# Optimization experiments

Measured on AMD Instinct MI355X. Metric: run time of the kernel, lower is better.

Reference implementation:

```python
import jax, jax.numpy as jnp
import numpy as np

D_IN = 1024
D_OUT = 1024
NUM_HEADS = 16
HEAD_DIM = D_OUT // NUM_HEADS
EPS = 1e-6
POW = 16.0


def setup_inputs() -> dict:
    key = jax.random.key(0)
    ks = jax.random.split(key, 6)
    s = 1.0 / np.sqrt(D_IN)
    x = jax.random.normal(ks[0], (2, 2048, D_IN), dtype=jnp.float32)
    Wq = jax.random.uniform(ks[1], (D_OUT, D_IN), jnp.float32, -s, s)
    Wk = jax.random.uniform(ks[2], (D_OUT, D_IN), jnp.float32, -s, s)
    Wv = jax.random.uniform(ks[3], (D_OUT, D_IN), jnp.float32, -s, s)
    Wo = jax.random.uniform(ks[4], (D_OUT, D_OUT), jnp.float32, -s, s)
    bo = jax.random.uniform(ks[5], (D_OUT,), jnp.float32, -s, s)
    return {"x": x, "Wq": Wq, "Wk": Wk, "Wv": Wv, "Wo": Wo, "bo": bo}


def _l2norm(t):
    # torch F.normalize: t / max(||t||, eps)
    n = jnp.sqrt(jnp.sum(t * t, axis=-1, keepdims=True))
    return t / jnp.maximum(n, EPS)


def reference(x, Wq, Wk, Wv, Wo, bo):
    B, T, _ = x.shape
    # project and split heads: [B, H, T, Dh]
    def heads(W):
        y = jnp.einsum('btd,od->bto', x, W)
        return y.reshape(B, T, NUM_HEADS, HEAD_DIM).transpose(0, 2, 1, 3)
    Q = _l2norm(heads(Wq))
    K = _l2norm(heads(Wk))
    V = heads(Wv)
    cos_sim = jnp.clip(jnp.einsum('bhtd,bhsd->bhts', Q, K), -0.999, 0.999)
    scores = 1.0 - jnp.arccos(cos_sim) / jnp.pi
    W = jnp.power(jnp.maximum(scores, EPS), POW)
    W = W / (jnp.sum(W, axis=-1, keepdims=True) + EPS)
    out = jnp.einsum('bhts,bhsd->bhtd', W, V)
    out = out.transpose(0, 2, 1, 3).reshape(B, T, D_OUT)
    return jnp.einsum('bto,po->btp', out, Wo) + bo
```

## Files before the change

### kernel.cpp

```cpp
#include <hip/hip_runtime.h>
#include <math.h>

constexpr int Dm   = 1024;
constexpr int NH   = 16;
constexpr int HD   = 64;
constexpr int Bb   = 2;
constexpr int Tt   = 2048;
constexpr int MTOT = Bb * Tt;
#define EPSF 1e-6f

typedef __attribute__((ext_vector_type(8))) short short8;
typedef __attribute__((ext_vector_type(4))) float f32x4;
typedef __attribute__((ext_vector_type(2))) float f32x2;

__device__ __forceinline__ ushort f2bf(float f) {
    union { float f; unsigned u; } v; v.f = f;
    unsigned r = (v.u + 0x7FFFu + ((v.u >> 16) & 1u)) >> 16;
    return (ushort)r;
}
__device__ __forceinline__ ushort f2bf_hu(float f) {
    return (ushort)((__builtin_bit_cast(unsigned, f) + 0x8000u) >> 16);
}

__device__ __forceinline__ void gload16(const void* g, void* l) {
    __builtin_amdgcn_global_load_lds(
        (const __attribute__((address_space(1))) unsigned int*)g,
        (__attribute__((address_space(3))) unsigned int*)l,
        16, 0, 0);
}

__global__ __launch_bounds__(256)
void cvt_all(const float* __restrict__ x,  const float* __restrict__ wq,
             const float* __restrict__ wk, const float* __restrict__ wv,
             const float* __restrict__ wo,
             ushort* __restrict__ xb,  ushort* __restrict__ wqb,
             ushort* __restrict__ wkb, ushort* __restrict__ wvb,
             ushort* __restrict__ wob) {
    int i = blockIdx.x * 256 + threadIdx.x;
    const float* src; ushort* dst; int off;
    if (i < 1048576)      { src = x;  dst = xb;  off = i; }
    else if (i < 1310720) { src = wq; dst = wqb; off = i - 1048576; }
    else if (i < 1572864) { src = wk; dst = wkb; off = i - 1310720; }
    else if (i < 1835008) { src = wv; dst = wvb; off = i - 1572864; }
    else                  { src = wo; dst = wob; off = i - 1835008; }
    const float4 v = ((const float4*)src)[off];
    ushort4 o;
    o.x = f2bf(v.x); o.y = f2bf(v.y); o.z = f2bf(v.z); o.w = f2bf(v.w);
    ((ushort4*)dst)[off] = o;
}

template<bool OUTF32>
__device__ __forceinline__
void gemm_core(const ushort* __restrict__ A, const ushort* __restrict__ W,
               const float* __restrict__ bias, void* __restrict__ out,
               int m0, int n0, int N, int K, int mode) {
    __shared__ ushort As[128 * 64];
    __shared__ ushort Bs[128 * 64];
    const int tid  = threadIdx.x;
    const int wave = tid >> 6, lane = tid & 63;
    const int quad = lane >> 4, l15 = lane & 15;
    const int wr = wave >> 1, wc = wave & 1;
    const int lr = lane >> 3;
    const int sc = (lane & 7) ^ lr;

    f32x4 acc[4][4] = {};
    const ushort* Ab = A + (size_t)(m0 + lr) * K + sc * 8;
    const ushort* Wb = W + (size_t)(n0 + lr) * K + sc * 8;

    for (int k0 = 0; k0 < K; k0 += 64) {
        #pragma unroll
        for (int i = 0; i < 4; i++) {
            const int rows8 = (wave * 4 + i) * 8;
            gload16(Ab + (size_t)rows8 * K + k0, &As[rows8 * 64]);
            gload16(Wb + (size_t)rows8 * K + k0, &Bs[rows8 * 64]);
        }
        __syncthreads();
        #pragma unroll
        for (int kh = 0; kh < 2; kh++) {
            short8 af[4];
            #pragma unroll
            for (int mi = 0; mi < 4; mi++) {
                const int row = wr * 64 + mi * 16 + l15;
                af[mi] = *(const short8*)&As[row * 64 + (((kh * 4 + quad) ^ (row & 7)) * 8)];
            }
            #pragma unroll
            for (int nj = 0; nj < 4; nj++) {
                const int row = wc * 64 + nj * 16 + l15;
                const short8 bf = *(const short8*)&Bs[row * 64 + (((kh * 4 + quad) ^ (row & 7)) * 8)];
                #pragma unroll
                for (int mi = 0; mi < 4; mi++)
                    acc[mi][nj] = __builtin_amdgcn_mfma_f32_16x16x32_bf16(af[mi], bf, acc[mi][nj], 0, 0, 0);
            }
        }
        __syncthreads();
    }

    if (!OUTF32 && mode == 2) {
        #pragma unroll
        for (int mi = 0; mi < 4; mi++) {
            const int t  = m0 + wr * 64 + mi * 16 + quad * 4;
            const int bb = t >> 11, tl = t & 2047;
            #pragma unroll
            for (int nj = 0; nj < 4; nj++) {
                const int n = n0 + wc * 64 + nj * 16 + l15;
                const int hh = n >> 6, dd = n & 63;
                uint2 pk;
                pk.x = (unsigned)f2bf(acc[mi][nj][0]) | ((unsigned)f2bf(acc[mi][nj][1]) << 16);
                pk.y = (unsigned)f2bf(acc[mi][nj][2]) | ((unsigned)f2bf(acc[mi][nj][3]) << 16);
                *(uint2*)&((ushort*)out)[(size_t)((bb * NH + hh) * HD + dd) * Tt + tl] = pk;
            }
        }
        return;
    }

    #pragma unroll
    for (int mi = 0; mi < 4; mi++) {
        float inv[4] = {1.f, 1.f, 1.f, 1.f};
        if (!OUTF32 && mode == 1) {
            #pragma unroll
            for (int r = 0; r < 4; r++) {
                float ss = 0.f;
                #pragma unroll
                for (int nj = 0; nj < 4; nj++) ss += acc[mi][nj][r] * acc[mi][nj][r];
                ss += __shfl_xor(ss, 1); ss += __shfl_xor(ss, 2);
                ss += __shfl_xor(ss, 4); ss += __shfl_xor(ss, 8);
                inv[r] = 1.f / fmaxf(sqrtf(ss), EPSF);
            }
        }
        #pragma unroll
        for (int nj = 0; nj < 4; nj++)
            #pragma unroll
            for (int r = 0; r < 4; r++) {
                const int row = m0 + wr * 64 + mi * 16 + quad * 4 + r;
                const int col = n0 + wc * 64 + nj * 16 + l15;
                if (OUTF32)
                    ((float*)out)[(size_t)row * N + col] = acc[mi][nj][r] + bias[col];
                else
                    ((ushort*)out)[(size_t)row * N + col] = f2bf(acc[mi][nj][r] * inv[r]);
            }
    }
}

__global__ __launch_bounds__(256)
void qkv_gemm(const ushort* __restrict__ xb,
              const ushort* __restrict__ wq, const ushort* __restrict__ wk,
              const ushort* __restrict__ wv,
              ushort* __restrict__ qb, ushort* __restrict__ kb,
              ushort* __restrict__ vtb) {
    const int ny = blockIdx.y, sel = ny >> 3;
    const ushort* W = (sel == 0) ? wq : (sel == 1) ? wk : wv;
    ushort* out     = (sel == 0) ? qb : (sel == 1) ? kb : vtb;
    gemm_core<false>(xb, W, nullptr, out, blockIdx.x * 128, (ny & 7) * 128,
                     Dm, Dm, (sel < 2) ? 1 : 2);
}

__global__ __launch_bounds__(256)
void out_gemm(const ushort* __restrict__ A, const ushort* __restrict__ W,
              const float* __restrict__ bias, float* __restrict__ out) {
    __shared__ ushort As[64 * 64];
    __shared__ ushort Bs[128 * 64];
    const int tid  = threadIdx.x;
    const int wave = tid >> 6, lane = tid & 63;
    const int quad = lane >> 4, l15 = lane & 15;
    const int wm = wave & 1, wn = wave >> 1;
    const int lr = lane >> 3;
    const int sc = (lane & 7) ^ lr;
    const int m0 = blockIdx.x * 64, n0 = blockIdx.y * 128;
    const int K = Dm, N = Dm;

    f32x4 acc[2][4] = {};
    const ushort* Ab = A + (size_t)(m0 + lr) * K + sc * 8;
    const ushort* Wb = W + (size_t)(n0 + lr) * K + sc * 8;

    for (int k0 = 0; k0 < K; k0 += 64) {
        #pragma unroll
        for (int i = 0; i < 2; i++) {
            const int rows8 = (wave * 2 + i) * 8;
            gload16(Ab + (size_t)rows8 * K + k0, &As[rows8 * 64]);
        }
        #pragma unroll
        for (int i = 0; i < 4; i++) {
            const int rows8 = (wave * 4 + i) * 8;
            gload16(Wb + (size_t)rows8 * K + k0, &Bs[rows8 * 64]);
        }
        __syncthreads();
        #pragma unroll
        for (int kh = 0; kh < 2; kh++) {
            short8 af[2];
            #pragma unroll
            for (int mi = 0; mi < 2; mi++) {
                const int row = wm * 32 + mi * 16 + l15;
                af[mi] = *(const short8*)&As[row * 64 + (((kh * 4 + quad) ^ (row & 7)) * 8)];
            }
            #pragma unroll
            for (int nj = 0; nj < 4; nj++) {
                const int row = wn * 64 + nj * 16 + l15;
                const short8 bf = *(const short8*)&Bs[row * 64 + (((kh * 4 + quad) ^ (row & 7)) * 8)];
                #pragma unroll
                for (int mi = 0; mi < 2; mi++)
                    acc[mi][nj] = __builtin_amdgcn_mfma_f32_16x16x32_bf16(af[mi], bf, acc[mi][nj], 0, 0, 0);
            }
        }
        __syncthreads();
    }
    #pragma unroll
    for (int mi = 0; mi < 2; mi++)
        #pragma unroll
        for (int nj = 0; nj < 4; nj++)
            #pragma unroll
            for (int r = 0; r < 4; r++) {
                const int row = m0 + wm * 32 + mi * 16 + quad * 4 + r;
                const int col = n0 + wn * 64 + nj * 16 + l15;
                out[(size_t)row * N + col] = acc[mi][nj][r] + bias[col];
            }
}

__global__ __launch_bounds__(256)
void attn_kernel(const ushort* __restrict__ Qb, const ushort* __restrict__ Kb,
                 const ushort* __restrict__ Vtb, ushort* __restrict__ Ob) {
    __shared__ ushort Ks[2][64 * 64];
    __shared__ ushort Vs[2][64 * 64];
    __shared__ ushort Ws[64 * 64];
    const int tid  = threadIdx.x;
    const int wave = tid >> 6, lane = tid & 63;
    const int quad = lane >> 4, l15 = lane & 15;
    const int t0 = blockIdx.x * 64, h = blockIdx.y, b = blockIdx.z;

    const size_t qrow = (size_t)(b * Tt + t0 + 16 * wave + l15) * Dm + h * HD;
    const short8 qf0 = *(const short8*)&Qb[qrow + quad * 8];
    const short8 qf1 = *(const short8*)&Qb[qrow + 32 + quad * 8];

    const size_t kbase  = (size_t)(b * Tt) * Dm + h * HD;
    const size_t vtbase = (size_t)((b * NH + h) * HD) * Tt;
    const int r0 = tid >> 3, ch0 = tid & 7;
    const ushort* kg = Kb  + kbase  + (size_t)r0 * Dm + ch0 * 8;
    const ushort* vg = Vtb + vtbase + (size_t)r0 * Tt + ch0 * 8;
    const int lsw0 = r0 * 64 + ((ch0 ^ (r0 & 7)) * 8);
    const int lsw1 = (r0 + 32) * 64 + ((ch0 ^ (r0 & 7)) * 8);

    f32x4 oacc[4] = {};
    f32x2 denp[4] = {};

    const f32x2 h3 = { 0.011180f,  0.011180f};
    const f32x2 h2 = {-0.002070f, -0.002070f};
    const f32x2 h1 = { 0.040732f,  0.040732f};
    const f32x2 h0 = { 0.450158f,  0.450158f};

    short8 pk0 = *(const short8*)kg;
    short8 pk1 = *(const short8*)(kg + (size_t)32 * Dm);
    short8 pv0 = *(const short8*)vg;
    short8 pv1 = *(const short8*)(vg + (size_t)32 * Tt);
    *(short8*)&Ks[0][lsw0] = pk0;  *(short8*)&Ks[0][lsw1] = pk1;
    *(short8*)&Vs[0][lsw0] = pv0;  *(short8*)&Vs[0][lsw1] = pv1;
    __syncthreads();

    for (int i = 0; i < 32; i++) {
        const int p = i & 1;
        if (i < 31) {
            const size_t sn = (size_t)(i + 1) * 64;
            pk0 = *(const short8*)(kg + sn * Dm);
            pk1 = *(const short8*)(kg + (sn + 32) * Dm);
            pv0 = *(const short8*)(vg + sn);
            pv1 = *(const short8*)(vg + sn + (size_t)32 * Tt);
        }

        f32x4 sf[4] = {};
        #pragma unroll
        for (int j = 0; j < 4; j++) {
            const int row = 16 * j + l15;
            const short8 kf0 = *(const short8*)&Ks[p][row * 64 + ((quad ^ (row & 7)) * 8)];
            const short8 kf1 = *(const short8*)&Ks[p][row * 64 + (((4 + quad) ^ (row & 7)) * 8)];
            sf[j] = __builtin_amdgcn_mfma_f32_16x16x32_bf16(qf0, kf0, sf[j], 0, 0, 0);
            sf[j] = __builtin_amdgcn_mfma_f32_16x16x32_bf16(qf1, kf1, sf[j], 0, 0, 0);
        }

        #pragma unroll
        for (int r = 0; r < 4; r++) {
            f32x2 tA, tB;
            tA.x = __builtin_amdgcn_fmed3f(1.0f - sf[0][r], 0.001f, 1.999f);
            tA.y = __builtin_amdgcn_fmed3f(1.0f - sf[1][r], 0.001f, 1.999f);
            tB.x = __builtin_amdgcn_fmed3f(1.0f - sf[2][r], 0.001f, 1.999f);
            tB.y = __builtin_amdgcn_fmed3f(1.0f - sf[3][r], 0.001f, 1.999f);
            f32x2 pa = __builtin_elementwise_fma(tA, h3, h2);
            f32x2 pb = __builtin_elementwise_fma(tB, h3, h2);
            pa = __builtin_elementwise_fma(pa, tA, h1);
            pb = __builtin_elementwise_fma(pb, tB, h1);
            pa = __builtin_elementwise_fma(pa, tA, h0);
            pb = __builtin_elementwise_fma(pb, tB, h0);
            f32x2 ra, rb;
            ra.x = __builtin_amdgcn_sqrtf(tA.x); ra.y = __builtin_amdgcn_sqrtf(tA.y);
            rb.x = __builtin_amdgcn_sqrtf(tB.x); rb.y = __builtin_amdgcn_sqrtf(tB.y);
            const f32x2 one2 = {1.0f, 1.0f};
            f32x2 wa = __builtin_elementwise_fma(-ra, pa, one2);
            f32x2 wb = __builtin_elementwise_fma(-rb, pb, one2);
            wa *= wa; wa *= wa; wa *= wa; wa *= wa;
            wb *= wb; wb *= wb; wb *= wb; wb *= wb;
            denp[r] += wa; denp[r] += wb;
            const int wrow = 16 * wave + quad * 4 + r;
            const int wb7 = wrow & 7;
            const int base = wrow * 64 + (l15 & 7);
            const int hc = l15 >> 3;
            Ws[base + (((hc)     ^ wb7) * 8)] = f2bf_hu(wa.x);
            Ws[base + (((hc + 2) ^ wb7) * 8)] = f2bf_hu(wa.y);
            Ws[base + (((hc + 4) ^ wb7) * 8)] = f2bf_hu(wb.x);
            Ws[base + (((hc + 6) ^ wb7) * 8)] = f2bf_hu(wb.y);
        }
        __syncthreads();

        const int wrow = 16 * wave + l15;
        const short8 wf0 = *(const short8*)&Ws[wrow * 64 + ((quad ^ (wrow & 7)) * 8)];
        const short8 wf1 = *(const short8*)&Ws[wrow * 64 + (((4 + quad) ^ (wrow & 7)) * 8)];
        #pragma unroll
        for (int j = 0; j < 4; j++) {
            const int vrow = 16 * j + l15;
            const short8 vf0 = *(const short8*)&Vs[p][vrow * 64 + ((quad ^ (vrow & 7)) * 8)];
            const short8 vf1 = *(const short8*)&Vs[p][vrow * 64 + (((4 + quad) ^ (vrow & 7)) * 8)];
            oacc[j] = __builtin_amdgcn_mfma_f32_16x16x32_bf16(wf0, vf0, oacc[j], 0, 0, 0);
            oacc[j] = __builtin_amdgcn_mfma_f32_16x16x32_bf16(wf1, vf1, oacc[j], 0, 0, 0);
        }
        if (i < 31) {
            *(short8*)&Ks[1 - p][lsw0] = pk0;  *(short8*)&Ks[1 - p][lsw1] = pk1;
            *(short8*)&Vs[1 - p][lsw0] = pv0;  *(short8*)&Vs[1 - p][lsw1] = pv1;
        }
        __syncthreads();
    }

    float den[4];
    #pragma unroll
    for (int r = 0; r < 4; r++) {
        float d = denp[r].x + denp[r].y;
        d += __shfl_xor(d, 1); d += __shfl_xor(d, 2);
        d += __shfl_xor(d, 4); d += __shfl_xor(d, 8);
        den[r] = __builtin_amdgcn_rcpf(d + EPSF);
    }
    const size_t obase =
        (size_t)(b * Tt + t0 + 16 * wave + quad * 4) * Dm + h * HD + l15;
    #pragma unroll
    for (int j = 0; j < 4; j++)
        #pragma unroll
        for (int r = 0; r < 4; r++)
            Ob[obase + (size_t)r * Dm + 16 * j] = f2bf(oacc[j][r] * den[r]);
}

extern "C" void kernel_launch(void* const* d_in, const int* in_sizes, int n_in,
                              void* d_out, int out_size, void* d_ws, size_t ws_size,
                              hipStream_t stream) {
    const float* x  = (const float*)d_in[0];
    const float* Wq = (const float*)d_in[1];
    const float* Wk = (const float*)d_in[2];
    const float* Wv = (const float*)d_in[3];
    const float* Wo = (const float*)d_in[4];
    const float* bo = (const float*)d_in[5];
    float* out = (float*)d_out;

    ushort* ws = (ushort*)d_ws;
    const size_t M1 = 1u << 20;
    ushort* xb  = ws;
    ushort* wqb = ws + 4 * M1;
    ushort* wkb = ws + 5 * M1;
    ushort* wvb = ws + 6 * M1;
    ushort* wob = ws + 7 * M1;
    ushort* qb  = ws + 8 * M1;
    ushort* kb  = ws + 12 * M1;
    ushort* vtb = ws + 16 * M1;
    ushort* aob = ws + 20 * M1;

    cvt_all<<<8192, 256, 0, stream>>>(x, Wq, Wk, Wv, Wo, xb, wqb, wkb, wvb, wob);
    qkv_gemm<<<dim3(MTOT / 128, 24), 256, 0, stream>>>(xb, wqb, wkb, wvb, qb, kb, vtb);
    attn_kernel<<<dim3(Tt / 64, NH, Bb), 256, 0, stream>>>(qb, kb, vtb, aob);
    out_gemm<<<dim3(MTOT / 64, Dm / 128), 256, 0, stream>>>(aob, wob, bo, out);
}
```

Baseline: 226.3 us.

## Keep attention weights in registers via transposed MFMA and permlane swaps

Computes the score tile transposed (K as the A operand) so each lane holds scores for one query row. The weights are then packed to bf16 with v_cvt_pk_bf16_f32 and rearranged through permlane32/16 swaps into B-operand fragments for the W·V MFMA. This removes the Ws shared-memory buffer, its scattered 16-bit stores and one __syncthreads per iteration, and it simplifies the denominator reduction and output stores into packed 8-byte writes. The risk is that the permlane fragment layout is wrong, and it relies on gfx950-specific instructions.

```diff
diff --git a/kernel.cpp b/kernel.cpp
--- a/kernel.cpp
+++ b/kernel.cpp
@@ -18,8 +18,11 @@
     unsigned r = (v.u + 0x7FFFu + ((v.u >> 16) & 1u)) >> 16;
     return (ushort)r;
 }
-__device__ __forceinline__ ushort f2bf_hu(float f) {
-    return (ushort)((__builtin_bit_cast(unsigned, f) + 0x8000u) >> 16);
+
+__device__ __forceinline__ unsigned cvt_pk_bf16(float lo, float hi) {
+    unsigned r;
+    asm("v_cvt_pk_bf16_f32 %0, %1, %2" : "=v"(r) : "v"(lo), "v"(hi));
+    return r;
 }
 
 __device__ __forceinline__ void gload16(const void* g, void* l) {
@@ -220,7 +223,6 @@
                  const ushort* __restrict__ Vtb, ushort* __restrict__ Ob) {
     __shared__ ushort Ks[2][64 * 64];
     __shared__ ushort Vs[2][64 * 64];
-    __shared__ ushort Ws[64 * 64];
     const int tid  = threadIdx.x;
     const int wave = tid >> 6, lane = tid & 63;
     const int quad = lane >> 4, l15 = lane & 15;
@@ -239,7 +241,7 @@
     const int lsw1 = (r0 + 32) * 64 + ((ch0 ^ (r0 & 7)) * 8);
 
     f32x4 oacc[4] = {};
-    f32x2 denp[4] = {};
+    f32x2 denp = {0.f, 0.f};
 
     const f32x2 h3 = { 0.011180f,  0.011180f};
     const f32x2 h2 = {-0.002070f, -0.002070f};
@@ -254,33 +256,38 @@
     *(short8*)&Vs[0][lsw0] = pv0;  *(short8*)&Vs[0][lsw1] = pv1;
     __syncthreads();
 
+    const ushort* kgp = kg + (size_t)64 * Dm;
+    const ushort* vgp = vg + 64;
+
     for (int i = 0; i < 32; i++) {
         const int p = i & 1;
         if (i < 31) {
-            const size_t sn = (size_t)(i + 1) * 64;
-            pk0 = *(const short8*)(kg + sn * Dm);
-            pk1 = *(const short8*)(kg + (sn + 32) * Dm);
-            pv0 = *(const short8*)(vg + sn);
-            pv1 = *(const short8*)(vg + sn + (size_t)32 * Tt);
-        }
-
-        f32x4 sf[4] = {};
+            pk0 = *(const short8*)kgp;
+            pk1 = *(const short8*)(kgp + (size_t)32 * Dm);
+            pv0 = *(const short8*)vgp;
+            pv1 = *(const short8*)(vgp + (size_t)32 * Tt);
+            kgp += (size_t)64 * Dm;
+            vgp += 64;
+        }
+
+        f32x4 sfT[4] = {};
         #pragma unroll
         for (int j = 0; j < 4; j++) {
             const int row = 16 * j + l15;
             const short8 kf0 = *(const short8*)&Ks[p][row * 64 + ((quad ^ (row & 7)) * 8)];
             const short8 kf1 = *(const short8*)&Ks[p][row * 64 + (((4 + quad) ^ (row & 7)) * 8)];
-            sf[j] = __builtin_amdgcn_mfma_f32_16x16x32_bf16(qf0, kf0, sf[j], 0, 0, 0);
-            sf[j] = __builtin_amdgcn_mfma_f32_16x16x32_bf16(qf1, kf1, sf[j], 0, 0, 0);
-        }
-
+            sfT[j] = __builtin_amdgcn_mfma_f32_16x16x32_bf16(kf0, qf0, sfT[j], 0, 0, 0);
+            sfT[j] = __builtin_amdgcn_mfma_f32_16x16x32_bf16(kf1, qf1, sfT[j], 0, 0, 0);
+        }
+
+        f32x2 wA[4], wB[4];
         #pragma unroll
         for (int r = 0; r < 4; r++) {
             f32x2 tA, tB;
-            tA.x = __builtin_amdgcn_fmed3f(1.0f - sf[0][r], 0.001f, 1.999f);
-            tA.y = __builtin_amdgcn_fmed3f(1.0f - sf[1][r], 0.001f, 1.999f);
-            tB.x = __builtin_amdgcn_fmed3f(1.0f - sf[2][r], 0.001f, 1.999f);
-            tB.y = __builtin_amdgcn_fmed3f(1.0f - sf[3][r], 0.001f, 1.999f);
+            tA.x = __builtin_amdgcn_fmed3f(1.0f - sfT[0][r], 0.001f, 1.999f);
+            tA.y = __builtin_amdgcn_fmed3f(1.0f - sfT[1][r], 0.001f, 1.999f);
+            tB.x = __builtin_amdgcn_fmed3f(1.0f - sfT[2][r], 0.001f, 1.999f);
+            tB.y = __builtin_amdgcn_fmed3f(1.0f - sfT[3][r], 0.001f, 1.999f);
             f32x2 pa = __builtin_elementwise_fma(tA, h3, h2);
             f32x2 pb = __builtin_elementwise_fma(tB, h3, h2);
             pa = __builtin_elementwise_fma(pa, tA, h1);
@@ -295,29 +302,40 @@
             f32x2 wb = __builtin_elementwise_fma(-rb, pb, one2);
             wa *= wa; wa *= wa; wa *= wa; wa *= wa;
             wb *= wb; wb *= wb; wb *= wb; wb *= wb;
-            denp[r] += wa; denp[r] += wb;
-            const int wrow = 16 * wave + quad * 4 + r;
-            const int wb7 = wrow & 7;
-            const int base = wrow * 64 + (l15 & 7);
-            const int hc = l15 >> 3;
-            Ws[base + (((hc)     ^ wb7) * 8)] = f2bf_hu(wa.x);
-            Ws[base + (((hc + 2) ^ wb7) * 8)] = f2bf_hu(wa.y);
-            Ws[base + (((hc + 4) ^ wb7) * 8)] = f2bf_hu(wb.x);
-            Ws[base + (((hc + 6) ^ wb7) * 8)] = f2bf_hu(wb.y);
-        }
-        __syncthreads();
-
-        const int wrow = 16 * wave + l15;
-        const short8 wf0 = *(const short8*)&Ws[wrow * 64 + ((quad ^ (wrow & 7)) * 8)];
-        const short8 wf1 = *(const short8*)&Ws[wrow * 64 + (((4 + quad) ^ (wrow & 7)) * 8)];
-        #pragma unroll
-        for (int j = 0; j < 4; j++) {
-            const int vrow = 16 * j + l15;
+            denp += wa; denp += wb;
+            wA[r] = wa; wB[r] = wb;
+        }
+
+        unsigned L0 = cvt_pk_bf16(wA[0].x, wA[1].x);
+        unsigned L1 = cvt_pk_bf16(wA[0].y, wA[1].y);
+        unsigned H0 = cvt_pk_bf16(wA[2].x, wA[3].x);
+        unsigned H1 = cvt_pk_bf16(wA[2].y, wA[3].y);
+        asm("v_permlane32_swap_b32 %0, %1" : "+v"(L0), "+v"(L1));
+        asm("v_permlane16_swap_b32 %0, %1" : "+v"(L0), "+v"(L1));
+        asm("v_permlane32_swap_b32 %0, %1" : "+v"(H0), "+v"(H1));
+        asm("v_permlane16_swap_b32 %0, %1" : "+v"(H0), "+v"(H1));
+        int4 bi1; bi1.x = (int)L0; bi1.y = (int)H0; bi1.z = (int)L1; bi1.w = (int)H1;
+        const short8 Bf1 = __builtin_bit_cast(short8, bi1);
+        unsigned L2 = cvt_pk_bf16(wB[0].x, wB[1].x);
+        unsigned L3 = cvt_pk_bf16(wB[0].y, wB[1].y);
+        unsigned H2 = cvt_pk_bf16(wB[2].x, wB[3].x);
+        unsigned H3 = cvt_pk_bf16(wB[2].y, wB[3].y);
+        asm("v_permlane32_swap_b32 %0, %1" : "+v"(L2), "+v"(L3));
+        asm("v_permlane16_swap_b32 %0, %1" : "+v"(L2), "+v"(L3));
+        asm("v_permlane32_swap_b32 %0, %1" : "+v"(H2), "+v"(H3));
+        asm("v_permlane16_swap_b32 %0, %1" : "+v"(H2), "+v"(H3));
+        int4 bi2; bi2.x = (int)L2; bi2.y = (int)H2; bi2.z = (int)L3; bi2.w = (int)H3;
+        const short8 Bf2 = __builtin_bit_cast(short8, bi2);
+
+        #pragma unroll
+        for (int jd = 0; jd < 4; jd++) {
+            const int vrow = 16 * jd + l15;
             const short8 vf0 = *(const short8*)&Vs[p][vrow * 64 + ((quad ^ (vrow & 7)) * 8)];
             const short8 vf1 = *(const short8*)&Vs[p][vrow * 64 + (((4 + quad) ^ (vrow & 7)) * 8)];
-            oacc[j] = __builtin_amdgcn_mfma_f32_16x16x32_bf16(wf0, vf0, oacc[j], 0, 0, 0);
-            oacc[j] = __builtin_amdgcn_mfma_f32_16x16x32_bf16(wf1, vf1, oacc[j], 0, 0, 0);
-        }
+            oacc[jd] = __builtin_amdgcn_mfma_f32_16x16x32_bf16(vf0, Bf1, oacc[jd], 0, 0, 0);
+            oacc[jd] = __builtin_amdgcn_mfma_f32_16x16x32_bf16(vf1, Bf2, oacc[jd], 0, 0, 0);
+        }
+
         if (i < 31) {
             *(short8*)&Ks[1 - p][lsw0] = pk0;  *(short8*)&Ks[1 - p][lsw1] = pk1;
             *(short8*)&Vs[1 - p][lsw0] = pv0;  *(short8*)&Vs[1 - p][lsw1] = pv1;
@@ -325,21 +343,19 @@
         __syncthreads();
     }
 
-    float den[4];
+    float d = denp.x + denp.y;
+    d += __shfl_xor(d, 16);
+    d += __shfl_xor(d, 32);
+    const float inv = __builtin_amdgcn_rcpf(d + EPSF);
+
+    const size_t orow = (size_t)(b * Tt + t0 + 16 * wave + l15) * Dm + h * HD;
     #pragma unroll
-    for (int r = 0; r < 4; r++) {
-        float d = denp[r].x + denp[r].y;
-        d += __shfl_xor(d, 1); d += __shfl_xor(d, 2);
-        d += __shfl_xor(d, 4); d += __shfl_xor(d, 8);
-        den[r] = __builtin_amdgcn_rcpf(d + EPSF);
-    }
-    const size_t obase =
-        (size_t)(b * Tt + t0 + 16 * wave + quad * 4) * Dm + h * HD + l15;
-    #pragma unroll
-    for (int j = 0; j < 4; j++)
-        #pragma unroll
-        for (int r = 0; r < 4; r++)
-            Ob[obase + (size_t)r * Dm + 16 * j] = f2bf(oacc[j][r] * den[r]);
+    for (int jd = 0; jd < 4; jd++) {
+        uint2 pk;
+        pk.x = cvt_pk_bf16(oacc[jd][0] * inv, oacc[jd][1] * inv);
+        pk.y = cvt_pk_bf16(oacc[jd][2] * inv, oacc[jd][3] * inv);
+        *(uint2*)&Ob[orow + 16 * jd + quad * 4] = pk;
+    }
 }
 
 extern "C" void kernel_launch(void* const* d_in, const int* in_sizes, int n_in,
```

Measured after the change: 219.7 us. 1.03x faster.
